# Performance work log

Measured on AMD Instinct MI355X. Metric: run time of the kernel, lower is better.

## Reference

```python
import jax, jax.numpy as jnp
import numpy as np

# Config (mirrors init_kwargs)
N_PARTS = 4
N_DATASETS = 4
N_VOLUMES = 12
N_TRANSFORMS = 1
TEMP = 0.1
EPS = 1e-6
BS = N_PARTS * N_DATASETS * N_VOLUMES          # 192
N = BS * (N_TRANSFORMS + 1)                    # 384 total rows
PD = N_PARTS * N_DATASETS                      # 16
C, H, W = 32, 48, 48


def setup_inputs() -> dict:
    key = jax.random.key(0)
    k1, k2 = jax.random.split(key)
    reg_pred = jax.random.normal(k1, (N, C, H, W), dtype=jnp.float32)
    mean_representations = jax.random.normal(k2, (N_DATASETS, C, H, W), dtype=jnp.float32)
    return {"reg_pred": reg_pred, "mean_representations": mean_representations}


def reference(reg_pred, mean_representations):
    X = reg_pred.reshape(N, -1)                                  # [N, D]
    ds_id = (jnp.arange(N) // N_PARTS) % N_DATASETS              # dataset id per row
    Mn = mean_representations.reshape(N_DATASETS, -1)[ds_id]     # [N, D] per-row mean
    Z = X - Mn                                                   # demeaned
    # cosine similarity with per-vector norm clamped at eps (torch CosineSimilarity)
    nrm = jnp.maximum(jnp.linalg.norm(Z, axis=1), EPS)
    Zn = Z / nrm[:, None]
    S = (Zn @ Zn.T) / TEMP                                       # [N, N] scaled cos sims
    E = jnp.exp(S)
    # negative (denominator) set for anchor a: all j with j % PD != a % PD
    rem = jnp.arange(N) % PD
    neg_mask = rem[:, None] != rem[None, :]
    Dsum = jnp.sum(E * neg_mask, axis=1)                         # [N]

    p = jnp.arange(BS)
    i1 = p
    i2 = BS + p
    i3 = (p + PD) % N
    i4 = (BS + p + PD) % N

    def pair_loss(a, b):
        # Faithful to original: BOTH terms use the (a,b) numerator similarity
        num = S[a, b]
        en = jnp.exp(num)
        return -(num - jnp.log(en + Dsum[a])) - (num - jnp.log(en + Dsum[b]))

    total = (pair_loss(i1, i2) + pair_loss(i3, i4)
             + pair_loss(i1, i3) + pair_loss(i2, i4)).sum()
    return total / (N_TRANSFORMS * 3 * BS)
```

## Files before the change

kernel.cpp:

```cpp
#include <hip/hip_runtime.h>
#include <hip/hip_bf16.h>
#include <stdint.h>

#define NR 384
#define DD 73728
#define PDV 16
#define BSV 192
#define KSPLIT 128
#define KCH 576
#define BK 64

typedef __bf16 bf16;
typedef __attribute__((ext_vector_type(8))) __bf16 bf16x8;
typedef __attribute__((ext_vector_type(4))) float f32x4;

__device__ __forceinline__ void async_copy16(const bf16* g, bf16* l) {
    __builtin_amdgcn_global_load_lds(
        (__attribute__((address_space(1))) void*)g,
        (__attribute__((address_space(3))) void*)l,
        16, 0, 0);
}

__global__ __launch_bounds__(256) void k_demean(const float* __restrict__ X,
                                                const float* __restrict__ M,
                                                bf16* __restrict__ Z) {
    int bx  = blockIdx.x;
    int row = bx / 36;
    int cb  = bx - row * 36;
    int col = (cb << 11) + (threadIdx.x << 3);
    int ds  = (row >> 2) & 3;
    size_t e = (size_t)row * DD + col;
    const float4* xp = (const float4*)(X + e);
    const float4* mp = (const float4*)(M + (size_t)ds * DD + col);
    float4 x0 = xp[0], x1 = xp[1];
    float4 m0 = mp[0], m1 = mp[1];
    bf16x8 z;
    z[0] = (bf16)(x0.x - m0.x);
    z[1] = (bf16)(x0.y - m0.y);
    z[2] = (bf16)(x0.z - m0.z);
    z[3] = (bf16)(x0.w - m0.w);
    z[4] = (bf16)(x1.x - m1.x);
    z[5] = (bf16)(x1.y - m1.y);
    z[6] = (bf16)(x1.z - m1.z);
    z[7] = (bf16)(x1.w - m1.w);
    *(bf16x8*)(Z + e) = z;
}

__global__ __launch_bounds__(256) void k_gram(const bf16* __restrict__ Z,
                                              float* __restrict__ Gp) {
    __shared__ bf16 ash[128 * BK];
    __shared__ bf16 bsh[128 * BK];
    const int tid  = threadIdx.x;
    const int lane = tid & 63;
    const int w    = tid >> 6;
    const int quad = lane >> 4;
    const int l15  = lane & 15;
    const int wm   = w & 1, wn = w >> 1;

    int bx   = blockIdx.x;
    int tile = bx % 6;
    int ks   = bx / 6;
    int tm = (tile < 3) ? 0 : ((tile < 5) ? 1 : 2);
    int tn = (tile < 3) ? tile : ((tile < 5) ? (tile - 2) : 2);
    int rowA0 = tm * 128, rowB0 = tn * 128;
    size_t k0 = (size_t)ks * KCH;

    f32x4 acc[4][4];
#pragma unroll
    for (int i = 0; i < 4; ++i)
#pragma unroll
        for (int j = 0; j < 4; ++j) acc[i][j] = (f32x4){0.f, 0.f, 0.f, 0.f};

    for (int kb = 0; kb < KCH; kb += BK) {
        size_t kbase = k0 + kb;
        __syncthreads();
#pragma unroll
        for (int t = 0; t < 4; ++t) {
            int S   = t * 256 + tid;
            int row = S >> 3;
            int sp  = S & 7;
            int gs  = sp ^ (row & 7);
            size_t gco = kbase + gs * 8;
            int ldsoff = (t * 256 + w * 64) * 8;
            async_copy16(Z + (size_t)(rowA0 + row) * DD + gco, &ash[ldsoff]);
            async_copy16(Z + (size_t)(rowB0 + row) * DD + gco, &bsh[ldsoff]);
        }
        __syncthreads();

#pragma unroll
        for (int kk = 0; kk < BK; kk += 32) {
            int sgi = (kk >> 5) * 4 + quad;
            bf16x8 af[4], bfv[4];
#pragma unroll
            for (int i = 0; i < 4; ++i) {
                int r = wm * 64 + i * 16 + l15;
                af[i] = *(const bf16x8*)&ash[r * BK + ((sgi ^ (r & 7)) << 3)];
            }
#pragma unroll
            for (int j = 0; j < 4; ++j) {
                int r = wn * 64 + j * 16 + l15;
                bfv[j] = *(const bf16x8*)&bsh[r * BK + ((sgi ^ (r & 7)) << 3)];
            }
#pragma unroll
            for (int i = 0; i < 4; ++i)
#pragma unroll
                for (int j = 0; j < 4; ++j)
                    acc[i][j] = __builtin_amdgcn_mfma_f32_16x16x32_bf16(
                        af[i], bfv[j], acc[i][j], 0, 0, 0);
        }
    }

    float* gp = Gp + ((size_t)(ks * 6 + tile) << 14);
#pragma unroll
    for (int i = 0; i < 4; ++i) {
        int lr0 = wm * 64 + i * 16 + quad * 4;
#pragma unroll
        for (int j = 0; j < 4; ++j) {
            int lc = wn * 64 + j * 16 + l15;
#pragma unroll
            for (int r = 0; r < 4; ++r)
                gp[(lr0 + r) * 128 + lc] = acc[i][j][r];
        }
    }
}

__global__ __launch_bounds__(256) void k_red(const float* __restrict__ Gp,
                                             float* __restrict__ G,
                                             float* __restrict__ invn) {
    int t    = blockIdx.x * 256 + threadIdx.x;
    int tile = t >> 14;
    int idx  = t & 16383;
    int lr   = idx >> 7, lc = idx & 127;
    const float* p = Gp + ((size_t)tile << 14) + idx;
    float s = 0.0f;
#pragma unroll 8
    for (int ks = 0; ks < KSPLIT; ++ks) s += p[(size_t)ks * 98304];
    int tm = (tile < 3) ? 0 : ((tile < 5) ? 1 : 2);
    int tn = (tile < 3) ? tile : ((tile < 5) ? (tile - 2) : 2);
    int a = tm * 128 + lr, b = tn * 128 + lc;
    G[(size_t)a * NR + b] = s;
    G[(size_t)b * NR + a] = s;
    if (a == b) invn[a] = 1.0f / fmaxf(sqrtf(s), 1e-6f);
}

__global__ __launch_bounds__(256) void k_dsum(const float* __restrict__ G,
                                              const float* __restrict__ invn,
                                              float* __restrict__ Ds) {
    const int lane = threadIdx.x & 63;
    const int a    = blockIdx.x * 4 + (threadIdx.x >> 6);
    float ia  = invn[a];
    int arem  = a & 15;
    float acc = 0.0f;
    for (int b = lane; b < NR; b += 64) {
        float s = G[(size_t)a * NR + b] * ia * invn[b] * 10.0f;
        if ((b & 15) != arem) acc += expf(s);
    }
#pragma unroll
    for (int o = 32; o > 0; o >>= 1) acc += __shfl_down(acc, o);
    if (lane == 0) Ds[a] = acc;
}

__device__ __forceinline__ float pairloss(const float* __restrict__ G,
                                          const float* __restrict__ invn,
                                          const float* __restrict__ Ds,
                                          int a, int b) {
    float num = G[(size_t)a * NR + b] * invn[a] * invn[b] * 10.0f;
    float en  = expf(num);
    return -(num - logf(en + Ds[a])) - (num - logf(en + Ds[b]));
}

__global__ __launch_bounds__(256) void k_final(const float* __restrict__ G,
                                               const float* __restrict__ invn,
                                               const float* __restrict__ Ds,
                                               float* __restrict__ out) {
    __shared__ float wred[4];
    const int tid  = threadIdx.x;
    const int lane = tid & 63;
    const int w    = tid >> 6;
    float c = 0.0f;
    if (tid < BSV) {
        int p = tid;
        int i1 = p, i2 = BSV + p;
        int i3 = (p + PDV) % NR, i4 = (BSV + p + PDV) % NR;
        c = pairloss(G, invn, Ds, i1, i2) + pairloss(G, invn, Ds, i3, i4)
          + pairloss(G, invn, Ds, i1, i3) + pairloss(G, invn, Ds, i2, i4);
    }
#pragma unroll
    for (int o = 32; o > 0; o >>= 1) c += __shfl_down(c, o);
    if (lane == 0) wred[w] = c;
    __syncthreads();
    if (tid == 0) {
        float tot = wred[0] + wred[1] + wred[2] + wred[3];
        out[0] = tot / 576.0f;
    }
}

extern "C" void kernel_launch(void* const* d_in, const int* in_sizes, int n_in,
                              void* d_out, int out_size, void* d_ws, size_t ws_size,
                              hipStream_t stream) {
    const float* X = (const float*)d_in[0];
    const float* M = (const float*)d_in[1];
    float* out = (float*)d_out;

    char* ws = (char*)d_ws;
    bf16*  Z    = (bf16*)ws;
    float* Gp   = (float*)(ws + (size_t)NR * DD * 2);
    float* G    = Gp + (size_t)KSPLIT * 6 * 16384;
    float* invn = G + (size_t)NR * NR;
    float* Ds   = invn + NR;

    k_demean<<<dim3(NR * 36), dim3(256), 0, stream>>>(X, M, Z);
    k_gram<<<dim3(6 * KSPLIT), dim3(256), 0, stream>>>(Z, Gp);
    k_red<<<dim3(384), dim3(256), 0, stream>>>(Gp, G, invn);
    k_dsum<<<dim3(NR / 4), dim3(256), 0, stream>>>(G, invn, Ds);
    k_final<<<dim3(1), dim3(256), 0, stream>>>(G, invn, Ds, out);
}
```

Measured before the change: 214.3 us.

## Fuse demean into gram loads and fold final loss into dsum

Drops the separate demean kernel and its bf16 Z buffer. The gram kernel now loads fp32 reg_pred tiles into LDS, subtracts the per-dataset mean (staged in LDS) in registers and converts to bf16 before the MFMAs, with BK halved to fit the fp32 tiles. The final pair-loss kernel is removed: each anchor's loss terms are computed in k_dsum and accumulated into the output with atomicAdd, and k_red zeroes the output first. The aim is to avoid the Z write and re-read and two launches, at the cost of twice the global and LDS bytes per gram K-step, more barriers per K, and extra VALU conversion work inside the GEMM loop.

Result: faster. 199.5 us (-6.9%).

```diff
diff --git a/kernel.cpp b/kernel.cpp
--- a/kernel.cpp
+++ b/kernel.cpp
@@ -8,53 +8,31 @@
 #define BSV 192
 #define KSPLIT 128
 #define KCH 576
-#define BK 64
+#define BK 32
 
 typedef __bf16 bf16;
 typedef __attribute__((ext_vector_type(8))) __bf16 bf16x8;
 typedef __attribute__((ext_vector_type(4))) float f32x4;
 
-__device__ __forceinline__ void async_copy16(const bf16* g, bf16* l) {
+__device__ __forceinline__ void async_copy16(const float* g, float* l) {
     __builtin_amdgcn_global_load_lds(
         (__attribute__((address_space(1))) void*)g,
         (__attribute__((address_space(3))) void*)l,
         16, 0, 0);
 }
 
-__global__ __launch_bounds__(256) void k_demean(const float* __restrict__ X,
-                                                const float* __restrict__ M,
-                                                bf16* __restrict__ Z) {
-    int bx  = blockIdx.x;
-    int row = bx / 36;
-    int cb  = bx - row * 36;
-    int col = (cb << 11) + (threadIdx.x << 3);
-    int ds  = (row >> 2) & 3;
-    size_t e = (size_t)row * DD + col;
-    const float4* xp = (const float4*)(X + e);
-    const float4* mp = (const float4*)(M + (size_t)ds * DD + col);
-    float4 x0 = xp[0], x1 = xp[1];
-    float4 m0 = mp[0], m1 = mp[1];
-    bf16x8 z;
-    z[0] = (bf16)(x0.x - m0.x);
-    z[1] = (bf16)(x0.y - m0.y);
-    z[2] = (bf16)(x0.z - m0.z);
-    z[3] = (bf16)(x0.w - m0.w);
-    z[4] = (bf16)(x1.x - m1.x);
-    z[5] = (bf16)(x1.y - m1.y);
-    z[6] = (bf16)(x1.z - m1.z);
-    z[7] = (bf16)(x1.w - m1.w);
-    *(bf16x8*)(Z + e) = z;
-}
-
-__global__ __launch_bounds__(256) void k_gram(const bf16* __restrict__ Z,
+__global__ __launch_bounds__(256) void k_gram(const float* __restrict__ X,
+                                              const float* __restrict__ M,
                                               float* __restrict__ Gp) {
-    __shared__ bf16 ash[128 * BK];
-    __shared__ bf16 bsh[128 * BK];
+    __shared__ float ashF[128 * BK];
+    __shared__ float bshF[128 * BK];
+    __shared__ float msh[4 * BK];
     const int tid  = threadIdx.x;
     const int lane = tid & 63;
     const int w    = tid >> 6;
     const int quad = lane >> 4;
     const int l15  = lane & 15;
+    const int l7   = lane & 7;
     const int wm   = w & 1, wn = w >> 1;
 
     int bx   = blockIdx.x;
@@ -80,34 +58,51 @@
             int row = S >> 3;
             int sp  = S & 7;
             int gs  = sp ^ (row & 7);
-            size_t gco = kbase + gs * 8;
-            int ldsoff = (t * 256 + w * 64) * 8;
-            async_copy16(Z + (size_t)(rowA0 + row) * DD + gco, &ash[ldsoff]);
-            async_copy16(Z + (size_t)(rowB0 + row) * DD + gco, &bsh[ldsoff]);
+            size_t gco = kbase + gs * 4;
+            int base = (t * 256 + w * 64) * 4;
+            async_copy16(X + (size_t)(rowA0 + row) * DD + gco, &ashF[base]);
+            async_copy16(X + (size_t)(rowB0 + row) * DD + gco, &bshF[base]);
+        }
+        if (tid < 32) {
+            float4 m4 = *(const float4*)(M + (size_t)(tid >> 3) * DD + kbase + (tid & 7) * 4);
+            *(float4*)&msh[tid * 4] = m4;
         }
         __syncthreads();
 
+        f32x4 mu = *(const f32x4*)&msh[(l15 >> 2) * BK + quad * 8];
+        f32x4 mv = *(const f32x4*)&msh[(l15 >> 2) * BK + quad * 8 + 4];
+
+        bf16x8 af[4], bfv[4];
 #pragma unroll
-        for (int kk = 0; kk < BK; kk += 32) {
-            int sgi = (kk >> 5) * 4 + quad;
-            bf16x8 af[4], bfv[4];
+        for (int i = 0; i < 4; ++i) {
+            int r = wm * 64 + i * 16 + l15;
+            f32x4 u = *(const f32x4*)&ashF[r * BK + (((quad << 1) ^ l7) << 2)];
+            f32x4 v = *(const f32x4*)&ashF[r * BK + ((((quad << 1) | 1) ^ l7) << 2)];
+            bf16x8 f;
+            f[0] = (bf16)(u[0] - mu[0]); f[1] = (bf16)(u[1] - mu[1]);
+            f[2] = (bf16)(u[2] - mu[2]); f[3] = (bf16)(u[3] - mu[3]);
+            f[4] = (bf16)(v[0] - mv[0]); f[5] = (bf16)(v[1] - mv[1]);
+            f[6] = (bf16)(v[2] - mv[2]); f[7] = (bf16)(v[3] - mv[3]);
+            af[i] = f;
+        }
 #pragma unroll
-            for (int i = 0; i < 4; ++i) {
-                int r = wm * 64 + i * 16 + l15;
-                af[i] = *(const bf16x8*)&ash[r * BK + ((sgi ^ (r & 7)) << 3)];
-            }
+        for (int j = 0; j < 4; ++j) {
+            int r = wn * 64 + j * 16 + l15;
+            f32x4 u = *(const f32x4*)&bshF[r * BK + (((quad << 1) ^ l7) << 2)];
+            f32x4 v = *(const f32x4*)&bshF[r * BK + ((((quad << 1) | 1) ^ l7) << 2)];
+            bf16x8 f;
+            f[0] = (bf16)(u[0] - mu[0]); f[1] = (bf16)(u[1] - mu[1]);
+            f[2] = (bf16)(u[2] - mu[2]); f[3] = (bf16)(u[3] - mu[3]);
+            f[4] = (bf16)(v[0] - mv[0]); f[5] = (bf16)(v[1] - mv[1]);
+            f[6] = (bf16)(v[2] - mv[2]); f[7] = (bf16)(v[3] - mv[3]);
+            bfv[j] = f;
+        }
 #pragma unroll
-            for (int j = 0; j < 4; ++j) {
-                int r = wn * 64 + j * 16 + l15;
-                bfv[j] = *(const bf16x8*)&bsh[r * BK + ((sgi ^ (r & 7)) << 3)];
-            }
+        for (int i = 0; i < 4; ++i)
 #pragma unroll
-            for (int i = 0; i < 4; ++i)
-#pragma unroll
-                for (int j = 0; j < 4; ++j)
-                    acc[i][j] = __builtin_amdgcn_mfma_f32_16x16x32_bf16(
-                        af[i], bfv[j], acc[i][j], 0, 0, 0);
-        }
+            for (int j = 0; j < 4; ++j)
+                acc[i][j] = __builtin_amdgcn_mfma_f32_16x16x32_bf16(
+                    af[i], bfv[j], acc[i][j], 0, 0, 0);
     }
 
     float* gp = Gp + ((size_t)(ks * 6 + tile) << 14);
@@ -126,8 +121,10 @@
 
 __global__ __launch_bounds__(256) void k_red(const float* __restrict__ Gp,
                                              float* __restrict__ G,
-                                             float* __restrict__ invn) {
+                                             float* __restrict__ invn,
+                                             float* __restrict__ out) {
     int t    = blockIdx.x * 256 + threadIdx.x;
+    if (t == 0) out[0] = 0.0f;
     int tile = t >> 14;
     int idx  = t & 16383;
     int lr   = idx >> 7, lc = idx & 127;
@@ -145,7 +142,7 @@
 
 __global__ __launch_bounds__(256) void k_dsum(const float* __restrict__ G,
                                               const float* __restrict__ invn,
-                                              float* __restrict__ Ds) {
+                                              float* __restrict__ out) {
     const int lane = threadIdx.x & 63;
     const int a    = blockIdx.x * 4 + (threadIdx.x >> 6);
     float ia  = invn[a];
@@ -157,41 +154,21 @@
     }
 #pragma unroll
     for (int o = 32; o > 0; o >>= 1) acc += __shfl_down(acc, o);
-    if (lane == 0) Ds[a] = acc;
-}
-
-__device__ __forceinline__ float pairloss(const float* __restrict__ G,
-                                          const float* __restrict__ invn,
-                                          const float* __restrict__ Ds,
-                                          int a, int b) {
-    float num = G[(size_t)a * NR + b] * invn[a] * invn[b] * 10.0f;
-    float en  = expf(num);
-    return -(num - logf(en + Ds[a])) - (num - logf(en + Ds[b]));
-}
-
-__global__ __launch_bounds__(256) void k_final(const float* __restrict__ G,
-                                               const float* __restrict__ invn,
-                                               const float* __restrict__ Ds,
-                                               float* __restrict__ out) {
-    __shared__ float wred[4];
-    const int tid  = threadIdx.x;
-    const int lane = tid & 63;
-    const int w    = tid >> 6;
-    float c = 0.0f;
-    if (tid < BSV) {
-        int p = tid;
-        int i1 = p, i2 = BSV + p;
-        int i3 = (p + PDV) % NR, i4 = (BSV + p + PDV) % NR;
-        c = pairloss(G, invn, Ds, i1, i2) + pairloss(G, invn, Ds, i3, i4)
-          + pairloss(G, invn, Ds, i1, i3) + pairloss(G, invn, Ds, i2, i4);
-    }
+    if (lane == 0) {
+        float Dsa = acc;
+        int pr[4];
+        if (a < 16)       { pr[0] = 192 + a; pr[1] = a + 16;  pr[2] = a + 192; pr[3] = a + 368; }
+        else if (a < 192) { pr[0] = 192 + a; pr[1] = a + 16;  pr[2] = a + 192; pr[3] = a - 16; }
+        else if (a < 368) { pr[0] = a - 192; pr[1] = a + 16;  pr[2] = a - 192; pr[3] = a - 16; }
+        else              { pr[0] = a - 192; pr[1] = a - 368; pr[2] = a - 192; pr[3] = a - 16; }
+        float t = 0.0f;
 #pragma unroll
-    for (int o = 32; o > 0; o >>= 1) c += __shfl_down(c, o);
-    if (lane == 0) wred[w] = c;
-    __syncthreads();
-    if (tid == 0) {
-        float tot = wred[0] + wred[1] + wred[2] + wred[3];
-        out[0] = tot / 576.0f;
+        for (int s = 0; s < 4; ++s) {
+            int b = pr[s];
+            float num = G[(size_t)a * NR + b] * ia * invn[b] * 10.0f;
+            t += -num + logf(expf(num) + Dsa);
+        }
+        atomicAdd(out, t * (1.0f / 576.0f));
     }
 }
 
@@ -203,15 +180,11 @@
     float* out = (float*)d_out;
 
     char* ws = (char*)d_ws;
-    bf16*  Z    = (bf16*)ws;
-    float* Gp   = (float*)(ws + (size_t)NR * DD * 2);
+    float* Gp   = (float*)ws;
     float* G    = Gp + (size_t)KSPLIT * 6 * 16384;
     float* invn = G + (size_t)NR * NR;
-    float* Ds   = invn + NR;
 
-    k_demean<<<dim3(NR * 36), dim3(256), 0, stream>>>(X, M, Z);
-    k_gram<<<dim3(6 * KSPLIT), dim3(256), 0, stream>>>(Z, Gp);
-    k_red<<<dim3(384), dim3(256), 0, stream>>>(Gp, G, invn);
-    k_dsum<<<dim3(NR / 4), dim3(256), 0, stream>>>(G, invn, Ds);
-    k_final<<<dim3(1), dim3(256), 0, stream>>>(G, invn, Ds, out);
+    k_gram<<<dim3(6 * KSPLIT), dim3(256), 0, stream>>>(X, M, Gp);
+    k_red<<<dim3(384), dim3(256), 0, stream>>>(Gp, G, invn, out);
+    k_dsum<<<dim3(NR / 4), dim3(256), 0, stream>>>(G, invn, out);
 }
```
